# Kernel optimization log

Measured on AMD Instinct MI355X. Metric: run time of the kernel, lower is better.

Reference implementation:

```python
import jax, jax.numpy as jnp
import numpy as np

B, T, L, H, NH, F, V, K = 8, 128, 12, 768, 12, 3072, 30522, 5
DH = H // NH
START, STOP = 3, 4  # tag_to_idx['<START>'], tag_to_idx['<STOP>']


def _ln(x, s, b):
    m = jnp.mean(x, -1, keepdims=True)
    v = jnp.var(x, -1, keepdims=True)
    return (x - m) * jax.lax.rsqrt(v + 1e-12) * s + b


def setup_inputs() -> dict:
    key = jax.random.key(0)
    ks = jax.random.split(key, 16)
    sc = 0.02
    rn = lambda k, shp: jax.random.normal(k, shp, jnp.float32) * sc
    inp = {
        'sentence': jax.random.randint(ks[0], (B, T), 0, V),
        'sentence_mask': jnp.ones((B, T), jnp.int32),
        'word_emb': rn(ks[1], (V, H)),
        'pos_emb': rn(ks[2], (T, H)),
        'type_emb': rn(ks[3], (2, H)),
        'emb_ln_s': jnp.ones((H,), jnp.float32),
        'emb_ln_b': jnp.zeros((H,), jnp.float32),
        'Wqkv': rn(ks[4], (L, H, 3 * H)), 'bqkv': jnp.zeros((L, 3 * H), jnp.float32),
        'Wo': rn(ks[5], (L, H, H)), 'bo': jnp.zeros((L, H), jnp.float32),
        'ln1_s': jnp.ones((L, H), jnp.float32), 'ln1_b': jnp.zeros((L, H), jnp.float32),
        'W1': rn(ks[6], (L, H, F)), 'b1': jnp.zeros((L, F), jnp.float32),
        'W2': rn(ks[7], (L, F, H)), 'b2': jnp.zeros((L, H), jnp.float32),
        'ln2_s': jnp.ones((L, H), jnp.float32), 'ln2_b': jnp.zeros((L, H), jnp.float32),
        'Wt': rn(ks[8], (H, K)), 'bt': jnp.zeros((K,), jnp.float32),
    }
    trans = jax.random.normal(ks[9], (K, K), jnp.float32)
    # transitions[START, :] = -10000 ; transitions[:, STOP] = -10000
    trans = trans.at[START, :].set(-10000.0).at[:, STOP].set(-10000.0)
    inp['transitions'] = trans
    return inp


def _bert_feats(sentence, sentence_mask, word_emb, pos_emb, type_emb,
                emb_ln_s, emb_ln_b, Wqkv, bqkv, Wo, bo, ln1_s, ln1_b,
                W1, b1, W2, b2, ln2_s, ln2_b, Wt, bt):
    # embeddings (token_type_ids=None -> all zeros)
    x = word_emb[sentence] + pos_emb[None, :, :] + type_emb[0][None, None, :]
    x = _ln(x, emb_ln_s, emb_ln_b)
    # additive attention bias from padding mask
    bias = (1.0 - sentence_mask.astype(jnp.float32))[:, None, None, :] * -10000.0
    inv_sqrt_dh = 1.0 / np.sqrt(DH)

    def layer(h, p):
        wqkv, bqk, wo, bo_, s1, sb1, w1, wb1, w2, wb2, s2, sb2 = p
        qkv = h @ wqkv + bqk
        q, k, v = jnp.split(qkv, 3, axis=-1)
        q = q.reshape(B, T, NH, DH)
        k = k.reshape(B, T, NH, DH)
        v = v.reshape(B, T, NH, DH)
        att = jnp.einsum('bqhd,bkhd->bhqk', q, k) * inv_sqrt_dh + bias
        att = jax.nn.softmax(att, axis=-1)
        ctx = jnp.einsum('bhqk,bkhd->bqhd', att, v).reshape(B, T, H)
        h = _ln(h + ctx @ wo + bo_, s1, sb1)
        ff = jax.nn.gelu(h @ w1 + wb1) @ w2 + wb2
        h = _ln(h + ff, s2, sb2)
        return h, None

    x, _ = jax.lax.scan(layer, x, (Wqkv, bqkv, Wo, bo, ln1_s, ln1_b,
                                   W1, b1, W2, b2, ln2_s, ln2_b))
    # dropout(p=0.2) is identity at inference
    return x @ Wt + bt  # [B, T, K]


def _viterbi(feats, transitions):
    # feats: [B, T, K]; transitions[to, from]
    init = jnp.full((B, K), -10000.0, feats.dtype).at[:, START].set(0.0)

    def fwd_step(ld, feat_t):
        m = transitions[None, :, :] + ld[:, None, :]  # [B, K(to), K(from)]
        best = jnp.max(m, axis=-1)
        psi_t = jnp.argmax(m, axis=-1)
        return best + feat_t, psi_t

    feats_t = jnp.swapaxes(feats, 0, 1)  # [T, B, K]
    ld, psis = jax.lax.scan(fwd_step, init, feats_t[1:])  # psis: [T-1, B, K]
    score = jnp.max(ld, axis=-1)          # [B]
    last = jnp.argmax(ld, axis=-1)        # [B]

    def bwd_step(p, psi_t):
        prev = jnp.take_along_axis(psi_t, p[:, None], axis=-1)[:, 0]
        return prev, prev

    _, rest = jax.lax.scan(bwd_step, last, psis, reverse=True)  # [T-1, B]
    path = jnp.concatenate([rest, last[None, :]], axis=0).T     # [B, T]
    return score, path


def reference(sentence, sentence_mask, word_emb, pos_emb, type_emb,
              emb_ln_s, emb_ln_b, Wqkv, bqkv, Wo, bo, ln1_s, ln1_b,
              W1, b1, W2, b2, ln2_s, ln2_b, Wt, bt, transitions):
    feats = _bert_feats(sentence, sentence_mask, word_emb, pos_emb, type_emb,
                        emb_ln_s, emb_ln_b, Wqkv, bqkv, Wo, bo, ln1_s, ln1_b,
                        W1, b1, W2, b2, ln2_s, ln2_b, Wt, bt)
    score, path = _viterbi(feats, transitions)
    return score, path
```

## Files before the change

kernel.cpp:

```cpp
#include <hip/hip_runtime.h>
#include <cstdint>
#include <cstddef>

#define BB 8
#define TT 128
#define LL 12
#define HH 768
#define NHH 12
#define DHH 64
#define FFI 3072
#define KT 5
#define START_TAG 3
#define MTOK (BB*TT)

#define LQS 1769472u
#define LOS 589824u
#define L1S 2359296u
#define L2S 2359296u

typedef _Float16 f16x8 __attribute__((ext_vector_type(8)));
typedef _Float16 f16x4 __attribute__((ext_vector_type(4)));
typedef float f32x4 __attribute__((ext_vector_type(4)));

__device__ __forceinline__ void gl_lds16(const _Float16* g, _Float16* l) {
    __builtin_amdgcn_global_load_lds(
        (const __attribute__((address_space(1))) unsigned int*)g,
        (__attribute__((address_space(3))) unsigned int*)l, 16, 0, 0);
}

__device__ __forceinline__ float gelu_f(float x) {
    float c = 0.7978845608028654f * (x + 0.044715f * x * x * x);
    return 0.5f * x * (1.f + tanhf(c));
}

__device__ __forceinline__ void write_h_planes(const float* rowbuf, int tok,
                                               _Float16* dh, _Float16* dl, int c) {
    int kb = c >> 2;
    int rowm = tok & 127, mb = tok >> 7;
    int koct = c & 3;
    int p = rowm * 4 + (koct ^ (rowm & 3));
    size_t tb = ((size_t)(mb * 24 + kb)) * 4096;
    f16x8 vh, vl;
#pragma unroll
    for (int j = 0; j < 8; ++j) {
        float x = rowbuf[c * 8 + j];
        _Float16 hi = (_Float16)x;
        vh[j] = hi;
        vl[j] = (_Float16)((x - (float)hi) * 4096.f);
    }
    *(f16x8*)(dh + tb + (size_t)p * 8) = vh;
    *(f16x8*)(dl + tb + (size_t)p * 8) = vl;
}

__global__ __launch_bounds__(256) void embed_ln_kernel(
    const int* __restrict__ sentence,
    const float* __restrict__ word_emb,
    const float* __restrict__ pos_emb,
    const float* __restrict__ type_emb,
    const float* __restrict__ ln_s,
    const float* __restrict__ ln_b,
    float* __restrict__ h,
    _Float16* __restrict__ dh, _Float16* __restrict__ dl)
{
    int tok = blockIdx.x;
    int t = tok % TT;
    int id = sentence[tok];
    const float* we = word_emb + (size_t)id * HH;
    const float* pe = pos_emb + (size_t)t * HH;

    __shared__ float rowbuf[HH];
    __shared__ float rs_[4], rss_[4];
    float x[3];
    float s = 0.f, ss = 0.f;
#pragma unroll
    for (int i = 0; i < 3; ++i) {
        int d = threadIdx.x + i * 256;
        float v = we[d] + pe[d] + type_emb[d];
        x[i] = v; s += v; ss += v * v;
    }
    for (int o = 32; o; o >>= 1) { s += __shfl_down(s, o); ss += __shfl_down(ss, o); }
    int wid = threadIdx.x >> 6;
    if ((threadIdx.x & 63) == 0) { rs_[wid] = s; rss_[wid] = ss; }
    __syncthreads();
    s = rs_[0] + rs_[1] + rs_[2] + rs_[3];
    ss = rss_[0] + rss_[1] + rss_[2] + rss_[3];
    float mean = s * (1.f / HH);
    float var = ss * (1.f / HH) - mean * mean;
    float rstd = rsqrtf(var + 1e-12f);
#pragma unroll
    for (int i = 0; i < 3; ++i) {
        int d = threadIdx.x + i * 256;
        float y = (x[i] - mean) * rstd * ln_s[d] + ln_b[d];
        h[(size_t)tok * HH + d] = y;
        rowbuf[d] = y;
    }
    __syncthreads();
    if (threadIdx.x < 96) write_h_planes(rowbuf, tok, dh, dl, threadIdx.x);
}

template<int FEATS>
__global__ __launch_bounds__(256) void add_ln_red_kernel(
    float* __restrict__ h, const float* __restrict__ parts,
    const float* __restrict__ bias,
    const float* __restrict__ ln_s, const float* __restrict__ ln_b,
    _Float16* __restrict__ dh, _Float16* __restrict__ dl,
    const float* __restrict__ Wt, const float* __restrict__ bt,
    float* __restrict__ feats)
{
    int tok = blockIdx.x;
    __shared__ float rowbuf[HH];
    __shared__ float rs_[4], rss_[4];
    float x[3];
    float s = 0.f, ss = 0.f;
#pragma unroll
    for (int i = 0; i < 3; ++i) {
        int d = threadIdx.x + i * 256;
        size_t idx = (size_t)tok * HH + d;
        float delta = parts[idx] + parts[idx + (size_t)MTOK * HH]
                    + parts[idx + 2 * (size_t)MTOK * HH] + parts[idx + 3 * (size_t)MTOK * HH]
                    + bias[d];
        float v = h[idx] + delta;
        x[i] = v; s += v; ss += v * v;
    }
    for (int o = 32; o; o >>= 1) { s += __shfl_down(s, o); ss += __shfl_down(ss, o); }
    int wid = threadIdx.x >> 6;
    if ((threadIdx.x & 63) == 0) { rs_[wid] = s; rss_[wid] = ss; }
    __syncthreads();
    s = rs_[0] + rs_[1] + rs_[2] + rs_[3];
    ss = rss_[0] + rss_[1] + rss_[2] + rss_[3];
    float mean = s * (1.f / HH);
    float var = ss * (1.f / HH) - mean * mean;
    float rstd = rsqrtf(var + 1e-12f);
    float yv[3];
#pragma unroll
    for (int i = 0; i < 3; ++i) {
        int d = threadIdx.x + i * 256;
        float y = (x[i] - mean) * rstd * ln_s[d] + ln_b[d];
        yv[i] = y;
        if constexpr (!FEATS) {
            h[(size_t)tok * HH + d] = y;
            rowbuf[d] = y;
        }
    }
    if constexpr (!FEATS) {
        __syncthreads();
        if (threadIdx.x < 96) write_h_planes(rowbuf, tok, dh, dl, threadIdx.x);
    } else {
        float pt[5] = {0.f, 0.f, 0.f, 0.f, 0.f};
#pragma unroll
        for (int i = 0; i < 3; ++i) {
            int d = threadIdx.x + i * 256;
#pragma unroll
            for (int t = 0; t < 5; ++t) pt[t] += yv[i] * Wt[d * 5 + t];
        }
#pragma unroll
        for (int t = 0; t < 5; ++t)
            for (int o = 32; o; o >>= 1) pt[t] += __shfl_down(pt[t], o);
        __shared__ float fred[4][5];
        if ((threadIdx.x & 63) == 0)
#pragma unroll
            for (int t = 0; t < 5; ++t) fred[wid][t] = pt[t];
        __syncthreads();
        if (threadIdx.x < 5) {
            float fs = fred[0][threadIdx.x] + fred[1][threadIdx.x]
                     + fred[2][threadIdx.x] + fred[3][threadIdx.x] + bt[threadIdx.x];
            feats[tok * 5 + threadIdx.x] = fs;
        }
    }
}

template<int ALL>
__global__ __launch_bounds__(256) void wconv_kernel(
    const float* __restrict__ Wqkv, const float* __restrict__ Wo,
    const float* __restrict__ W1, const float* __restrict__ W2,
    _Float16* __restrict__ qh, _Float16* __restrict__ ql,
    _Float16* __restrict__ oh, _Float16* __restrict__ ol,
    _Float16* __restrict__ f1h, _Float16* __restrict__ f1l,
    _Float16* __restrict__ f2h, _Float16* __restrict__ f2l)
{
    int bb = blockIdx.x;
    int l = ALL ? bb / 3456 : 0;
    int b = ALL ? bb % 3456 : bb;
    const float* src; _Float16 *dh, *dl; int N, kTi, idx;
    if (b < 864)       { idx = b;        src = Wqkv + (size_t)l * 768 * 2304; dh = qh  + (size_t)l * LQS; dl = ql  + (size_t)l * LQS; N = 2304; kTi = 24; }
    else if (b < 1152) { idx = b - 864;  src = Wo   + (size_t)l * 768 * 768;  dh = oh  + (size_t)l * LOS; dl = ol  + (size_t)l * LOS; N = 768;  kTi = 24; }
    else if (b < 2304) { idx = b - 1152; src = W1   + (size_t)l * 768 * 3072; dh = f1h + (size_t)l * L1S; dl = f1l + (size_t)l * L1S; N = 3072; kTi = 24; }
    else               { idx = b - 2304; src = W2   + (size_t)l * 3072 * 768; dh = f2h + (size_t)l * L2S; dl = f2l + (size_t)l * L2S; N = 768;  kTi = 96; }
    int nb = idx / kTi, kb = idx % kTi;

    __shared__ float tile[32][65];
    const float* s0 = src + (size_t)(kb * 32) * N + nb * 64;
#pragma unroll
    for (int i = 0; i < 8; ++i) {
        int q = threadIdx.x + i * 256;
        int kk = q >> 6, n = q & 63;
        tile[kk][n] = s0[(size_t)kk * N + n];
    }
    __syncthreads();
    int p = threadIdx.x;
    int n = p >> 2, koct = (p & 3) ^ (n & 3);
    f16x8 vh, vl;
#pragma unroll
    for (int j = 0; j < 8; ++j) {
        float x = tile[koct * 8 + j][n];
        _Float16 hi = (_Float16)x;
        vh[j] = hi;
        vl[j] = (_Float16)((x - (float)hi) * 4096.f);
    }
    size_t tb = (size_t)idx * 2048;
    *(f16x8*)(dh + tb + (size_t)p * 8) = vh;
    *(f16x8*)(dl + tb + (size_t)p * 8) = vl;
}

template<int MODE>
__global__ __launch_bounds__(256) void mfma_gemm(
    const _Float16* __restrict__ Ah, const _Float16* __restrict__ Al,
    const _Float16* __restrict__ Bh, const _Float16* __restrict__ Bl,
    const float* __restrict__ bias, float* __restrict__ outF,
    _Float16* __restrict__ o1h, _Float16* __restrict__ o1l,
    _Float16* __restrict__ o2h, _Float16* __restrict__ o2l,
    int N, int kTi, int kpz)
{
    constexpr bool TRANS = (MODE >= 2);
    __shared__ _Float16 lds[2][12288];
    int tid = threadIdx.x, lane = tid & 63, w = tid >> 6;
    int wm = w >> 1, wn = w & 1;
    int mb = blockIdx.y, nb = blockIdx.x;
    int ktBeg = TRANS ? 0 : blockIdx.z * kpz;
    int ktEnd = TRANS ? kTi : ktBeg + kpz;

    const _Float16 *aTh, *aTl, *bTh, *bTl;
    if constexpr (!TRANS) {
        aTh = Ah + (size_t)mb * kTi * 4096;
        aTl = Al + (size_t)mb * kTi * 4096;
        bTh = Bh + (size_t)nb * kTi * 2048;
        bTl = Bl + (size_t)nb * kTi * 2048;
    } else {
        aTh = Ah + (size_t)(2 * mb) * kTi * 2048;
        aTl = Al + (size_t)(2 * mb) * kTi * 2048;
        bTh = Bh + (size_t)(nb >> 1) * kTi * 4096 + (nb & 1) * 2048;
        bTl = Bl + (size_t)(nb >> 1) * kTi * 4096 + (nb & 1) * 2048;
    }

    f32x4 acch[4][2], accc[4][2];
#pragma unroll
    for (int i = 0; i < 4; ++i)
#pragma unroll
        for (int j = 0; j < 2; ++j) { acch[i][j] = (f32x4)0.f; accc[i][j] = (f32x4)0.f; }

    auto stage = [&](int buf, int kt) {
#pragma unroll
        for (int j = 0; j < 6; ++j) {
            int i = w * 6 + j;
            const _Float16* src;
            if constexpr (!TRANS) {
                if (i < 8)       src = aTh + (size_t)kt * 4096 + i * 512;
                else if (i < 16) src = aTl + (size_t)kt * 4096 + (i - 8) * 512;
                else if (i < 20) src = bTh + (size_t)kt * 2048 + (i - 16) * 512;
                else             src = bTl + (size_t)kt * 2048 + (i - 20) * 512;
            } else {
                if (i < 8)       src = aTh + (size_t)(i >> 2) * kTi * 2048 + (size_t)kt * 2048 + (i & 3) * 512;
                else if (i < 16) src = aTl + (size_t)((i - 8) >> 2) * kTi * 2048 + (size_t)kt * 2048 + ((i - 8) & 3) * 512;
                else if (i < 20) src = bTh + (size_t)kt * 4096 + (i - 16) * 512;
                else             src = bTl + (size_t)kt * 4096 + (i - 20) * 512;
            }
            gl_lds16(src + lane * 8, &lds[buf][i * 512]);
        }
    };

    stage(0, ktBeg);
    __syncthreads();
    int buf = 0;
    int lm = lane & 15, lk = lane >> 4;
    for (int kt = ktBeg; kt < ktEnd; ++kt) {
        if (kt + 1 < ktEnd) stage(buf ^ 1, kt + 1);
        const char* lb = (const char*)&lds[buf][0];
        f16x8 ahf[4], alf[4], bhf[2], blf[2];
#pragma unroll
        for (int mi = 0; mi < 4; ++mi) {
            int row = wm * 64 + mi * 16 + lm;
            int off = (row * 64 + lk * 16) ^ ((row & 3) << 4);
            ahf[mi] = *(const f16x8*)(lb + off);
            alf[mi] = *(const f16x8*)(lb + 8192 + off);
        }
#pragma unroll
        for (int ni = 0; ni < 2; ++ni) {
            int nr = wn * 32 + ni * 16 + lm;
            int off = (nr * 64 + lk * 16) ^ ((nr & 3) << 4);
            bhf[ni] = *(const f16x8*)(lb + 16384 + off);
            blf[ni] = *(const f16x8*)(lb + 20480 + off);
        }
#pragma unroll
        for (int mi = 0; mi < 4; ++mi)
#pragma unroll
            for (int ni = 0; ni < 2; ++ni) {
                acch[mi][ni] = __builtin_amdgcn_mfma_f32_16x16x32_f16(ahf[mi], bhf[ni], acch[mi][ni], 0, 0, 0);
                accc[mi][ni] = __builtin_amdgcn_mfma_f32_16x16x32_f16(ahf[mi], blf[ni], accc[mi][ni], 0, 0, 0);
                accc[mi][ni] = __builtin_amdgcn_mfma_f32_16x16x32_f16(alf[mi], bhf[ni], accc[mi][ni], 0, 0, 0);
            }
        __syncthreads();
        buf ^= 1;
    }

    const float inv = 1.0f / 4096.0f;
    if constexpr (MODE == 0) {
        float* Cz = outF + (size_t)blockIdx.z * 1024 * N;
#pragma unroll
        for (int mi = 0; mi < 4; ++mi)
#pragma unroll
            for (int ni = 0; ni < 2; ++ni) {
                int col = nb * 64 + wn * 32 + ni * 16 + lm;
                int r0 = mb * 128 + wm * 64 + mi * 16 + lk * 4;
#pragma unroll
                for (int j = 0; j < 4; ++j)
                    Cz[(size_t)(r0 + j) * N + col] = acch[mi][ni][j] + accc[mi][ni][j] * inv;
            }
    } else if constexpr (MODE == 2) {
        int region = mb / 6;
#pragma unroll
        for (int mi = 0; mi < 4; ++mi)
#pragma unroll
            for (int ni = 0; ni < 2; ++ni) {
                int n = mb * 128 + wm * 64 + mi * 16 + lk * 4;
                int tok = nb * 64 + wn * 32 + ni * 16 + lm;
                float4 bv = *(const float4*)(bias + n);
                float v[4];
#pragma unroll
                for (int j = 0; j < 4; ++j)
                    v[j] = acch[mi][ni][j] + accc[mi][ni][j] * inv + (&bv.x)[j];
                int b = tok >> 7, q = tok & 127;
                if (region < 2) {
                    int hh2 = (n >> 6) % 12, d = n & 63;
                    size_t img = (size_t)(b * 12 + hh2);
                    _Float16* dsth = (region == 0) ? o1h : o2h;
                    _Float16* dstl = (region == 0) ? o1l : o2l;
                    int byteo = q * 128 + ((d * 2) ^ ((q & 7) << 4));
                    f16x4 hi, lo;
#pragma unroll
                    for (int j = 0; j < 4; ++j) {
                        _Float16 hv = (_Float16)v[j];
                        hi[j] = hv; lo[j] = (_Float16)((v[j] - (float)hv) * 4096.f);
                    }
                    *(f16x4*)((char*)dsth + img * 16384 + byteo) = hi;
                    *(f16x4*)((char*)dstl + img * 16384 + byteo) = lo;
                } else {
                    int hh2 = (n - 1536) >> 6, d = n & 63;
                    float* vdst = outF + (size_t)(b * 12 + hh2) * 8192;
#pragma unroll
                    for (int j = 0; j < 4; ++j)
                        vdst[(size_t)(d + j) * 128 + q] = v[j];
                }
            }
    } else {
#pragma unroll
        for (int mi = 0; mi < 4; ++mi)
#pragma unroll
            for (int ni = 0; ni < 2; ++ni) {
                int n = mb * 128 + wm * 64 + mi * 16 + lk * 4;
                int tok = nb * 64 + wn * 32 + ni * 16 + lm;
                float4 bv = *(const float4*)(bias + n);
                int mbt = tok >> 7, rowm = tok & 127;
                int kb = n >> 5, koct = (n >> 3) & 3, half = (n >> 2) & 1;
                size_t eo = ((size_t)(mbt * 96 + kb)) * 4096
                          + (size_t)(rowm * 4 + (koct ^ (rowm & 3))) * 8 + half * 4;
                f16x4 hi, lo;
#pragma unroll
                for (int j = 0; j < 4; ++j) {
                    float x = gelu_f(acch[mi][ni][j] + accc[mi][ni][j] * inv + (&bv.x)[j]);
                    _Float16 hv = (_Float16)x;
                    hi[j] = hv; lo[j] = (_Float16)((x - (float)hv) * 4096.f);
                }
                *(f16x4*)(o1h + eo) = hi;
                *(f16x4*)(o1l + eo) = lo;
            }
    }
}

__global__ __launch_bounds__(256, 2) void attn_mfma(
    const _Float16* __restrict__ Qp_h, const _Float16* __restrict__ Qp_l,
    const _Float16* __restrict__ Kp_h, const _Float16* __restrict__ Kp_l,
    const float* __restrict__ vT, const int* __restrict__ mask,
    _Float16* __restrict__ cA_h, _Float16* __restrict__ cA_l)
{
    __shared__ __align__(16) char sm[81920];
    char* Kh  = sm;             char* Klo = sm + 16384;
    char* Qh  = sm + 32768;     char* Qlo = sm + 40960;
    char* Ph  = sm;             char* Plo = sm + 16384;
    char* Vth = sm + 49152;     char* Vtl = sm + 65536;

    int bx = blockIdx.x;
    int bh = bx >> 1, qh2 = bx & 1;
    int b = bh / 12, h = bh % 12;
    int q0 = qh2 * 64;
    int tid = threadIdx.x, lane = tid & 63, wv = tid >> 6;
    int lm = lane & 15, g = lane >> 4;
    int qr = wv * 16 + lm;
    const float inv = 1.0f / 4096.0f;

    {
        const _Float16* Ksh = Kp_h + (size_t)bh * 8192;
        const _Float16* Ksl = Kp_l + (size_t)bh * 8192;
        const _Float16* Qsh = Qp_h + (size_t)bh * 8192 + (size_t)q0 * 64;
        const _Float16* Qsl = Qp_l + (size_t)bh * 8192 + (size_t)q0 * 64;
#pragma unroll
        for (int i = 0; i < 4; ++i) {
            gl_lds16(Ksh + (size_t)(i * 256 + tid) * 8, (_Float16*)(Kh  + (i * 256 + tid) * 16));
            gl_lds16(Ksl + (size_t)(i * 256 + tid) * 8, (_Float16*)(Klo + (i * 256 + tid) * 16));
        }
#pragma unroll
        for (int i = 0; i < 2; ++i) {
            gl_lds16(Qsh + (size_t)(i * 256 + tid) * 8, (_Float16*)(Qh  + (i * 256 + tid) * 16));
            gl_lds16(Qsl + (size_t)(i * 256 + tid) * 8, (_Float16*)(Qlo + (i * 256 + tid) * 16));
        }
    }
    float kb_[8][4];
    {
        const int* mrow = mask + b * 128;
#pragma unroll
        for (int mf = 0; mf < 8; ++mf) {
            int4 mv = *(const int4*)(mrow + mf * 16 + g * 4);
            kb_[mf][0] = (1.f - (float)mv.x) * -10000.f;
            kb_[mf][1] = (1.f - (float)mv.y) * -10000.f;
            kb_[mf][2] = (1.f - (float)mv.z) * -10000.f;
            kb_[mf][3] = (1.f - (float)mv.w) * -10000.f;
        }
    }
    __syncthreads();

    f32x4 ah[8], ac[8];
#pragma unroll
    for (int i = 0; i < 8; ++i) { ah[i] = (f32x4)0.f; ac[i] = (f32x4)0.f; }
    __builtin_amdgcn_s_setprio(1);
#pragma unroll
    for (int ks = 0; ks < 2; ++ks) {
        int qoff = qr * 128 + ((ks * 64 + g * 16) ^ ((qr & 7) << 4));
        f16x8 q_h = *(const f16x8*)(Qh + qoff);
        f16x8 q_l = *(const f16x8*)(Qlo + qoff);
#pragma unroll
        for (int mf = 0; mf < 8; ++mf) {
            int kt = mf * 16 + lm;
            int koff = kt * 128 + ((ks * 64 + g * 16) ^ ((kt & 7) << 4));
            f16x8 k_h = *(const f16x8*)(Kh + koff);
            f16x8 k_l = *(const f16x8*)(Klo + koff);
            ah[mf] = __builtin_amdgcn_mfma_f32_16x16x32_f16(k_h, q_h, ah[mf], 0, 0, 0);
            ac[mf] = __builtin_amdgcn_mfma_f32_16x16x32_f16(k_h, q_l, ac[mf], 0, 0, 0);
            ac[mf] = __builtin_amdgcn_mfma_f32_16x16x32_f16(k_l, q_h, ac[mf], 0, 0, 0);
        }
    }
    __builtin_amdgcn_s_setprio(0);

    float pv_[8][4];
    float mx = -1e30f;
#pragma unroll
    for (int mf = 0; mf < 8; ++mf)
#pragma unroll
        for (int jj = 0; jj < 4; ++jj) {
            float s = (ah[mf][jj] + ac[mf][jj] * inv) * 0.125f + kb_[mf][jj];
            pv_[mf][jj] = s;
            mx = fmaxf(mx, s);
        }
    mx = fmaxf(mx, __shfl_xor(mx, 16));
    mx = fmaxf(mx, __shfl_xor(mx, 32));
    float sum = 0.f;
#pragma unroll
    for (int mf = 0; mf < 8; ++mf)
#pragma unroll
        for (int jj = 0; jj < 4; ++jj) {
            float e = expf(pv_[mf][jj] - mx);
            pv_[mf][jj] = e;
            sum += e;
        }
    sum += __shfl_xor(sum, 16);
    sum += __shfl_xor(sum, 32);
    float rs = 1.f / sum;
    __syncthreads();

#pragma unroll
    for (int mf = 0; mf < 8; ++mf) {
        f16x4 hi, lo;
#pragma unroll
        for (int jj = 0; jj < 4; ++jj) {
            float p = pv_[mf][jj] * rs;
            _Float16 hv = (_Float16)p;
            hi[jj] = hv; lo[jj] = (_Float16)((p - (float)hv) * 4096.f);
        }
        int byteo = qr * 256 + ((mf * 32 + g * 8) ^ ((qr & 7) << 4));
        *(f16x4*)(Ph + byteo) = hi;
        *(f16x4*)(Plo + byteo) = lo;
    }
    {
        int d = tid >> 2, tb = (tid & 3) * 32;
        const float* vsrc = vT + (size_t)bh * 8192 + (size_t)d * 128 + tb;
#pragma unroll
        for (int i = 0; i < 8; ++i) {
            float4 v = *(const float4*)(vsrc + i * 4);
            f16x4 hi, lo;
#pragma unroll
            for (int jj = 0; jj < 4; ++jj) {
                float x = (&v.x)[jj];
                _Float16 hv = (_Float16)x;
                hi[jj] = hv; lo[jj] = (_Float16)((x - (float)hv) * 4096.f);
            }
            int byteo = d * 256 + (((tb + i * 4) * 2) ^ ((d & 7) << 4));
            *(f16x4*)(Vth + byteo) = hi;
            *(f16x4*)(Vtl + byteo) = lo;
        }
    }
    __syncthreads();

    f32x4 ch[4], cc[4];
#pragma unroll
    for (int i = 0; i < 4; ++i) { ch[i] = (f32x4)0.f; cc[i] = (f32x4)0.f; }
    __builtin_amdgcn_s_setprio(1);
#pragma unroll
    for (int ks = 0; ks < 4; ++ks) {
        int poff = qr * 256 + ((ks * 64 + g * 16) ^ ((qr & 7) << 4));
        f16x8 p_h = *(const f16x8*)(Ph + poff);
        f16x8 p_l = *(const f16x8*)(Plo + poff);
#pragma unroll
        for (int mf = 0; mf < 4; ++mf) {
            int d = mf * 16 + lm;
            int voff = d * 256 + ((ks * 64 + g * 16) ^ ((d & 7) << 4));
            f16x8 vh = *(const f16x8*)(Vth + voff);
            f16x8 vl = *(const f16x8*)(Vtl + voff);
            ch[mf] = __builtin_amdgcn_mfma_f32_16x16x32_f16(vh, p_h, ch[mf], 0, 0, 0);
            cc[mf] = __builtin_amdgcn_mfma_f32_16x16x32_f16(vh, p_l, cc[mf], 0, 0, 0);
            cc[mf] = __builtin_amdgcn_mfma_f32_16x16x32_f16(vl, p_h, cc[mf], 0, 0, 0);
        }
    }
    __builtin_amdgcn_s_setprio(0);

    int q = q0 + qr;
#pragma unroll
    for (int mf = 0; mf < 4; ++mf) {
        int d0 = mf * 16 + g * 4;
        f16x4 hi, lo;
#pragma unroll
        for (int jj = 0; jj < 4; ++jj) {
            float x = ch[mf][jj] + cc[mf][jj] * inv;
            _Float16 hv = (_Float16)x;
            hi[jj] = hv; lo[jj] = (_Float16)((x - (float)hv) * 4096.f);
        }
        int kb = h * 2 + (d0 >> 5), koct = (d0 >> 3) & 3, half = (d0 >> 2) & 1;
        size_t eo = ((size_t)(b * 24 + kb)) * 4096
                  + (size_t)(q * 4 + (koct ^ (q & 3))) * 8 + half * 4;
        *(f16x4*)(cA_h + eo) = hi;
        *(f16x4*)(cA_l + eo) = lo;
    }
}

__global__ __launch_bounds__(64) void viterbi_kernel(
    const float* __restrict__ feats, const float* __restrict__ trans,
    float* __restrict__ out)
{
    __shared__ float tr[KT][KT];
    __shared__ unsigned char psi[TT - 1][BB][KT];
    int tid = threadIdx.x;
    if (tid < KT * KT) tr[tid / KT][tid % KT] = trans[tid];
    __syncthreads();
    if (tid < BB) {
        int b = tid;
        float ld[KT];
#pragma unroll
        for (int k = 0; k < KT; ++k) ld[k] = (k == START_TAG) ? 0.f : -10000.f;
        for (int t = 1; t < TT; ++t) {
            float nld[KT];
#pragma unroll
            for (int to = 0; to < KT; ++to) {
                float best = tr[to][0] + ld[0];
                int arg = 0;
#pragma unroll
                for (int fr = 1; fr < KT; ++fr) {
                    float v = tr[to][fr] + ld[fr];
                    if (v > best) { best = v; arg = fr; }
                }
                psi[t - 1][b][to] = (unsigned char)arg;
                nld[to] = best + feats[(size_t)(b * TT + t) * KT + to];
            }
#pragma unroll
            for (int k = 0; k < KT; ++k) ld[k] = nld[k];
        }
        float sc = ld[0]; int last = 0;
#pragma unroll
        for (int k = 1; k < KT; ++k) if (ld[k] > sc) { sc = ld[k]; last = k; }
        out[b] = sc;
        int p = last;
        out[BB + b * TT + (TT - 1)] = (float)last;
        for (int t = TT - 2; t >= 0; --t) {
            p = psi[t][b][p];
            out[BB + b * TT + t] = (float)p;
        }
    }
}

extern "C" void kernel_launch(void* const* d_in, const int* in_sizes, int n_in,
                              void* d_out, int out_size, void* d_ws, size_t ws_size,
                              hipStream_t stream) {
    const int*   sentence = (const int*)d_in[0];
    const int*   mask     = (const int*)d_in[1];
    const float* word_emb = (const float*)d_in[2];
    const float* pos_emb  = (const float*)d_in[3];
    const float* type_emb = (const float*)d_in[4];
    const float* emb_ln_s = (const float*)d_in[5];
    const float* emb_ln_b = (const float*)d_in[6];
    const float* Wqkv     = (const float*)d_in[7];
    const float* bqkv     = (const float*)d_in[8];
    const float* Wo       = (const float*)d_in[9];
    const float* bo       = (const float*)d_in[10];
    const float* ln1_s    = (const float*)d_in[11];
    const float* ln1_b    = (const float*)d_in[12];
    const float* W1       = (const float*)d_in[13];
    const float* b1       = (const float*)d_in[14];
    const float* W2       = (const float*)d_in[15];
    const float* b2       = (const float*)d_in[16];
    const float* ln2_s    = (const float*)d_in[17];
    const float* ln2_b    = (const float*)d_in[18];
    const float* Wt       = (const float*)d_in[19];
    const float* bt       = (const float*)d_in[20];
    const float* trans    = (const float*)d_in[21];

    char* base = (char*)d_ws;
    size_t off = 0;
    auto alloc = [&](size_t bytes) { void* p = base + off; off += (bytes + 255) & ~(size_t)255; return p; };

    bool allL = ws_size >= (384ULL << 20);
    int NLL = allL ? 12 : 1;

    _Float16* wq_h = (_Float16*)alloc((size_t)LQS * NLL * 2);
    _Float16* wq_l = (_Float16*)alloc((size_t)LQS * NLL * 2);
    _Float16* wo_h = (_Float16*)alloc((size_t)LOS * NLL * 2);
    _Float16* wo_l = (_Float16*)alloc((size_t)LOS * NLL * 2);
    _Float16* w1_h = (_Float16*)alloc((size_t)L1S * NLL * 2);
    _Float16* w1_l = (_Float16*)alloc((size_t)L1S * NLL * 2);
    _Float16* w2_h = (_Float16*)alloc((size_t)L2S * NLL * 2);
    _Float16* w2_l = (_Float16*)alloc((size_t)L2S * NLL * 2);
    float* h       = (float*)alloc((size_t)MTOK * HH * 4);
    _Float16* hA_h = (_Float16*)alloc((size_t)MTOK * HH * 2);
    _Float16* hA_l = (_Float16*)alloc((size_t)MTOK * HH * 2);
    _Float16* Qp_h = (_Float16*)alloc((size_t)96 * 8192 * 2);
    _Float16* Qp_l = (_Float16*)alloc((size_t)96 * 8192 * 2);
    _Float16* Kp_h = (_Float16*)alloc((size_t)96 * 8192 * 2);
    _Float16* Kp_l = (_Float16*)alloc((size_t)96 * 8192 * 2);
    float* vT      = (float*)alloc((size_t)96 * 8192 * 4);
    _Float16* cA_h = (_Float16*)alloc((size_t)MTOK * HH * 2);
    _Float16* cA_l = (_Float16*)alloc((size_t)MTOK * HH * 2);
    _Float16* gA_h = (_Float16*)alloc((size_t)MTOK * FFI * 2);
    _Float16* gA_l = (_Float16*)alloc((size_t)MTOK * FFI * 2);
    float* parts   = (float*)alloc((size_t)4 * MTOK * HH * 4);
    float* featsb  = (float*)alloc((size_t)MTOK * KT * 4);

    embed_ln_kernel<<<MTOK, 256, 0, stream>>>(sentence, word_emb, pos_emb, type_emb,
                                              emb_ln_s, emb_ln_b, h, hA_h, hA_l);
    if (allL) {
        wconv_kernel<1><<<41472, 256, 0, stream>>>(
            Wqkv, Wo, W1, W2, wq_h, wq_l, wo_h, wo_l, w1_h, w1_l, w2_h, w2_l);
    }
    for (int l = 0; l < LL; ++l) {
        size_t qO  = allL ? (size_t)l * LQS : 0;
        size_t oO  = allL ? (size_t)l * LOS : 0;
        size_t f1O = allL ? (size_t)l * L1S : 0;
        size_t f2O = allL ? (size_t)l * L2S : 0;
        if (!allL) {
            wconv_kernel<0><<<3456, 256, 0, stream>>>(
                Wqkv + (size_t)l * 768 * 2304, Wo + (size_t)l * 768 * 768,
                W1 + (size_t)l * 768 * 3072, W2 + (size_t)l * 3072 * 768,
                wq_h, wq_l, wo_h, wo_l, w1_h, w1_l, w2_h, w2_l);
        }
        mfma_gemm<2><<<dim3(16, 18), 256, 0, stream>>>(
            wq_h + qO, wq_l + qO, hA_h, hA_l, bqkv + (size_t)l * 2304, vT,
            Qp_h, Qp_l, Kp_h, Kp_l, 2304, 24, 24);
        attn_mfma<<<192, 256, 0, stream>>>(Qp_h, Qp_l, Kp_h, Kp_l, vT, mask, cA_h, cA_l);
        mfma_gemm<0><<<dim3(12, 8, 4), 256, 0, stream>>>(
            cA_h, cA_l, wo_h + oO, wo_l + oO, nullptr, parts,
            nullptr, nullptr, nullptr, nullptr, 768, 24, 6);
        add_ln_red_kernel<0><<<MTOK, 256, 0, stream>>>(
            h, parts, bo + (size_t)l * HH, ln1_s + (size_t)l * HH, ln1_b + (size_t)l * HH,
            hA_h, hA_l, nullptr, nullptr, nullptr);
        mfma_gemm<3><<<dim3(16, 24), 256, 0, stream>>>(
            w1_h + f1O, w1_l + f1O, hA_h, hA_l, b1 + (size_t)l * FFI, nullptr,
            gA_h, gA_l, nullptr, nullptr, 3072, 24, 24);
        mfma_gemm<0><<<dim3(12, 8, 4), 256, 0, stream>>>(
            gA_h, gA_l, w2_h + f2O, w2_l + f2O, nullptr, parts,
            nullptr, nullptr, nullptr, nullptr, 768, 96, 24);
        if (l < LL - 1) {
            add_ln_red_kernel<0><<<MTOK, 256, 0, stream>>>(
                h, parts, b2 + (size_t)l * HH, ln2_s + (size_t)l * HH, ln2_b + (size_t)l * HH,
                hA_h, hA_l, nullptr, nullptr, nullptr);
        } else {
            add_ln_red_kernel<1><<<MTOK, 256, 0, stream>>>(
                h, parts, b2 + (size_t)l * HH, ln2_s + (size_t)l * HH, ln2_b + (size_t)l * HH,
                hA_h, hA_l, Wt, bt, featsb);
        }
    }
    viterbi_kernel<<<1, 64, 0, stream>>>(featsb, trans, (float*)d_out);
}
```

Baseline: 1.630 ms.

## Enlarge GEMM block tile to 128x128 and halve grid sizes

The split-fp16 MFMA GEMM block tile grows from 128x64 to 128x128. Each wave now holds a 4x4 accumulator grid, LDS stages grow accordingly, and every GEMM launch uses half as many blocks along N. This raises arithmetic intensity and operand reuse per LDS load, but doubles accumulator registers and halves block count, e.g. QKV goes from 288 to 144 blocks and Wo/W2 from 384 to 192 on a 256-CU part, which risks underfilling the GPU. Launch bounds also change: GEMM now requests 2 blocks/SM and attention 1.

```diff
diff --git a/kernel.cpp b/kernel.cpp
--- a/kernel.cpp
+++ b/kernel.cpp
@@ -213,7 +213,7 @@
 }
 
 template<int MODE>
-__global__ __launch_bounds__(256) void mfma_gemm(
+__global__ __launch_bounds__(256, 2) void mfma_gemm(
     const _Float16* __restrict__ Ah, const _Float16* __restrict__ Al,
     const _Float16* __restrict__ Bh, const _Float16* __restrict__ Bl,
     const float* __restrict__ bias, float* __restrict__ outF,
@@ -222,47 +222,38 @@
     int N, int kTi, int kpz)
 {
     constexpr bool TRANS = (MODE >= 2);
-    __shared__ _Float16 lds[2][12288];
+    __shared__ _Float16 lds[2][16384];
     int tid = threadIdx.x, lane = tid & 63, w = tid >> 6;
     int wm = w >> 1, wn = w & 1;
     int mb = blockIdx.y, nb = blockIdx.x;
     int ktBeg = TRANS ? 0 : blockIdx.z * kpz;
     int ktEnd = TRANS ? kTi : ktBeg + kpz;
 
-    const _Float16 *aTh, *aTl, *bTh, *bTl;
-    if constexpr (!TRANS) {
-        aTh = Ah + (size_t)mb * kTi * 4096;
-        aTl = Al + (size_t)mb * kTi * 4096;
-        bTh = Bh + (size_t)nb * kTi * 2048;
-        bTl = Bl + (size_t)nb * kTi * 2048;
-    } else {
-        aTh = Ah + (size_t)(2 * mb) * kTi * 2048;
-        aTl = Al + (size_t)(2 * mb) * kTi * 2048;
-        bTh = Bh + (size_t)(nb >> 1) * kTi * 4096 + (nb & 1) * 2048;
-        bTl = Bl + (size_t)(nb >> 1) * kTi * 4096 + (nb & 1) * 2048;
-    }
-
-    f32x4 acch[4][2], accc[4][2];
+    f32x4 acch[4][4], accc[4][4];
 #pragma unroll
     for (int i = 0; i < 4; ++i)
 #pragma unroll
-        for (int j = 0; j < 2; ++j) { acch[i][j] = (f32x4)0.f; accc[i][j] = (f32x4)0.f; }
+        for (int j = 0; j < 4; ++j) { acch[i][j] = (f32x4)0.f; accc[i][j] = (f32x4)0.f; }
 
     auto stage = [&](int buf, int kt) {
 #pragma unroll
-        for (int j = 0; j < 6; ++j) {
-            int i = w * 6 + j;
+        for (int j = 0; j < 8; ++j) {
+            int i = w * 8 + j;
             const _Float16* src;
             if constexpr (!TRANS) {
-                if (i < 8)       src = aTh + (size_t)kt * 4096 + i * 512;
-                else if (i < 16) src = aTl + (size_t)kt * 4096 + (i - 8) * 512;
-                else if (i < 20) src = bTh + (size_t)kt * 2048 + (i - 16) * 512;
-                else             src = bTl + (size_t)kt * 2048 + (i - 20) * 512;
+                if (i < 8)       src = Ah + (size_t)mb * kTi * 4096 + (size_t)kt * 4096 + i * 512;
+                else if (i < 16) src = Al + (size_t)mb * kTi * 4096 + (size_t)kt * 4096 + (i - 8) * 512;
+                else if (i < 24) { int t = (i - 16) >> 2;
+                                   src = Bh + (size_t)(nb * 2 + t) * kTi * 2048 + (size_t)kt * 2048 + ((i - 16) & 3) * 512; }
+                else             { int t = (i - 24) >> 2;
+                                   src = Bl + (size_t)(nb * 2 + t) * kTi * 2048 + (size_t)kt * 2048 + ((i - 24) & 3) * 512; }
             } else {
-                if (i < 8)       src = aTh + (size_t)(i >> 2) * kTi * 2048 + (size_t)kt * 2048 + (i & 3) * 512;
-                else if (i < 16) src = aTl + (size_t)((i - 8) >> 2) * kTi * 2048 + (size_t)kt * 2048 + ((i - 8) & 3) * 512;
-                else if (i < 20) src = bTh + (size_t)kt * 4096 + (i - 16) * 512;
-                else             src = bTl + (size_t)kt * 4096 + (i - 20) * 512;
+                if (i < 8)       { int t = i >> 2;
+                                   src = Ah + (size_t)(2 * mb + t) * kTi * 2048 + (size_t)kt * 2048 + (i & 3) * 512; }
+                else if (i < 16) { int t = (i - 8) >> 2;
+                                   src = Al + (size_t)(2 * mb + t) * kTi * 2048 + (size_t)kt * 2048 + ((i - 8) & 3) * 512; }
+                else if (i < 24) src = Bh + (size_t)nb * kTi * 4096 + (size_t)kt * 4096 + (i - 16) * 512;
+                else             src = Bl + (size_t)nb * kTi * 4096 + (size_t)kt * 4096 + (i - 24) * 512;
             }
             gl_lds16(src + lane * 8, &lds[buf][i * 512]);
         }
@@ -275,7 +266,7 @@
     for (int kt = ktBeg; kt < ktEnd; ++kt) {
         if (kt + 1 < ktEnd) stage(buf ^ 1, kt + 1);
         const char* lb = (const char*)&lds[buf][0];
-        f16x8 ahf[4], alf[4], bhf[2], blf[2];
+        f16x8 ahf[4], alf[4], bhf[4], blf[4];
 #pragma unroll
         for (int mi = 0; mi < 4; ++mi) {
             int row = wm * 64 + mi * 16 + lm;
@@ -284,16 +275,22 @@
             alf[mi] = *(const f16x8*)(lb + 8192 + off);
         }
 #pragma unroll
-        for (int ni = 0; ni < 2; ++ni) {
-            int nr = wn * 32 + ni * 16 + lm;
-            int off = (nr * 64 + lk * 16) ^ ((nr & 3) << 4);
-            bhf[ni] = *(const f16x8*)(lb + 16384 + off);
-            blf[ni] = *(const f16x8*)(lb + 20480 + off);
+        for (int ni = 0; ni < 4; ++ni) {
+            int offb;
+            if constexpr (!TRANS) {
+                int nr = ni * 16 + lm;
+                offb = wn * 4096 + ((nr * 64 + lk * 16) ^ ((nr & 3) << 4));
+            } else {
+                int nr2 = wn * 64 + ni * 16 + lm;
+                offb = (nr2 * 64 + lk * 16) ^ ((nr2 & 3) << 4);
+            }
+            bhf[ni] = *(const f16x8*)(lb + 16384 + offb);
+            blf[ni] = *(const f16x8*)(lb + 24576 + offb);
         }
 #pragma unroll
         for (int mi = 0; mi < 4; ++mi)
 #pragma unroll
-            for (int ni = 0; ni < 2; ++ni) {
+            for (int ni = 0; ni < 4; ++ni) {
                 acch[mi][ni] = __builtin_amdgcn_mfma_f32_16x16x32_f16(ahf[mi], bhf[ni], acch[mi][ni], 0, 0, 0);
                 accc[mi][ni] = __builtin_amdgcn_mfma_f32_16x16x32_f16(ahf[mi], blf[ni], accc[mi][ni], 0, 0, 0);
                 accc[mi][ni] = __builtin_amdgcn_mfma_f32_16x16x32_f16(alf[mi], bhf[ni], accc[mi][ni], 0, 0, 0);
@@ -308,8 +305,8 @@
 #pragma unroll
         for (int mi = 0; mi < 4; ++mi)
 #pragma unroll
-            for (int ni = 0; ni < 2; ++ni) {
-                int col = nb * 64 + wn * 32 + ni * 16 + lm;
+            for (int ni = 0; ni < 4; ++ni) {
+                int col = nb * 128 + wn * 64 + ni * 16 + lm;
                 int r0 = mb * 128 + wm * 64 + mi * 16 + lk * 4;
 #pragma unroll
                 for (int j = 0; j < 4; ++j)
@@ -320,9 +317,9 @@
 #pragma unroll
         for (int mi = 0; mi < 4; ++mi)
 #pragma unroll
-            for (int ni = 0; ni < 2; ++ni) {
+            for (int ni = 0; ni < 4; ++ni) {
                 int n = mb * 128 + wm * 64 + mi * 16 + lk * 4;
-                int tok = nb * 64 + wn * 32 + ni * 16 + lm;
+                int tok = nb * 128 + wn * 64 + ni * 16 + lm;
                 float4 bv = *(const float4*)(bias + n);
                 float v[4];
 #pragma unroll
@@ -355,9 +352,9 @@
 #pragma unroll
         for (int mi = 0; mi < 4; ++mi)
 #pragma unroll
-            for (int ni = 0; ni < 2; ++ni) {
+            for (int ni = 0; ni < 4; ++ni) {
                 int n = mb * 128 + wm * 64 + mi * 16 + lk * 4;
-                int tok = nb * 64 + wn * 32 + ni * 16 + lm;
+                int tok = nb * 128 + wn * 64 + ni * 16 + lm;
                 float4 bv = *(const float4*)(bias + n);
                 int mbt = tok >> 7, rowm = tok & 127;
                 int kb = n >> 5, koct = (n >> 3) & 3, half = (n >> 2) & 1;
@@ -376,7 +373,7 @@
     }
 }
 
-__global__ __launch_bounds__(256, 2) void attn_mfma(
+__global__ __launch_bounds__(256, 1) void attn_mfma(
     const _Float16* __restrict__ Qp_h, const _Float16* __restrict__ Qp_l,
     const _Float16* __restrict__ Kp_h, const _Float16* __restrict__ Kp_l,
     const float* __restrict__ vT, const int* __restrict__ mask,
@@ -666,20 +663,20 @@
                 W1 + (size_t)l * 768 * 3072, W2 + (size_t)l * 3072 * 768,
                 wq_h, wq_l, wo_h, wo_l, w1_h, w1_l, w2_h, w2_l);
         }
-        mfma_gemm<2><<<dim3(16, 18), 256, 0, stream>>>(
+        mfma_gemm<2><<<dim3(8, 18), 256, 0, stream>>>(
             wq_h + qO, wq_l + qO, hA_h, hA_l, bqkv + (size_t)l * 2304, vT,
             Qp_h, Qp_l, Kp_h, Kp_l, 2304, 24, 24);
         attn_mfma<<<192, 256, 0, stream>>>(Qp_h, Qp_l, Kp_h, Kp_l, vT, mask, cA_h, cA_l);
-        mfma_gemm<0><<<dim3(12, 8, 4), 256, 0, stream>>>(
+        mfma_gemm<0><<<dim3(6, 8, 4), 256, 0, stream>>>(
             cA_h, cA_l, wo_h + oO, wo_l + oO, nullptr, parts,
             nullptr, nullptr, nullptr, nullptr, 768, 24, 6);
         add_ln_red_kernel<0><<<MTOK, 256, 0, stream>>>(
             h, parts, bo + (size_t)l * HH, ln1_s + (size_t)l * HH, ln1_b + (size_t)l * HH,
             hA_h, hA_l, nullptr, nullptr, nullptr);
-        mfma_gemm<3><<<dim3(16, 24), 256, 0, stream>>>(
+        mfma_gemm<3><<<dim3(8, 24), 256, 0, stream>>>(
             w1_h + f1O, w1_l + f1O, hA_h, hA_l, b1 + (size_t)l * FFI, nullptr,
             gA_h, gA_l, nullptr, nullptr, 3072, 24, 24);
-        mfma_gemm<0><<<dim3(12, 8, 4), 256, 0, stream>>>(
+        mfma_gemm<0><<<dim3(6, 8, 4), 256, 0, stream>>>(
             gA_h, gA_l, w2_h + f2O, w2_l + f2O, nullptr, parts,
             nullptr, nullptr, nullptr, nullptr, 768, 96, 24);
         if (l < LL - 1) {
```

New measurement: 1.807 ms. 1.11x slower.
